# Kernel tuning notes

Hardware: AMD Instinct MI355X
Metric: run time of the kernel (lower is better)

## Reference

```python
import jax, jax.numpy as jnp
import numpy as np

N = 50000      # nodes
M = 600000     # message edges (rows of e2)
E = 1600000    # bond-graph edges
H = 128        # hidden_channels
OE = 256       # out_emb_channels
OC = 1         # out_channels
NL = 3         # num_output_layers
ED = 8         # edge_dim


def _glorot(key, shape):
    fan_in = shape[-1]
    return jax.random.normal(key, shape, jnp.float32) / jnp.sqrt(jnp.float32(fan_in))


def setup_inputs() -> dict:
    key = jax.random.key(0)
    ks = jax.random.split(key, 24)
    inp = {}
    inp["e2"] = jax.random.normal(ks[0], (M, H), jnp.float32)
    inp["i"] = jax.random.randint(ks[1], (M,), 0, N)
    inp["afe"] = jax.random.normal(ks[2], (N, 7), jnp.float32)
    inp["b_edge_index"] = jax.random.randint(ks[3], (2, E), 0, N)
    inp["b_edge_attr"] = jax.random.uniform(ks[4], (E, ED), jnp.float32)
    # lin_v: Linear(H+7, H)
    inp["lin_v_w"] = _glorot(ks[5], (H, H + 7))
    inp["lin_v_b"] = jnp.zeros((H,), jnp.float32)
    # PDNConv (shared across both calls): lin (no bias) + edge MLP 8->8->1
    inp["conv_lin_w"] = _glorot(ks[6], (H, H))
    inp["mlp_w1"] = _glorot(ks[7], (ED, ED))
    inp["mlp_b1"] = jnp.zeros((ED,), jnp.float32)
    inp["mlp_w2"] = _glorot(ks[8], (1, ED))
    inp["mlp_b2"] = jnp.zeros((1,), jnp.float32)
    # lin_up: Linear(H, OE)
    inp["lin_up_w"] = _glorot(ks[9], (OE, H))
    inp["lin_up_b"] = jnp.zeros((OE,), jnp.float32)
    # output MLP stack: NL x Linear(OE, OE)
    inp["lins_w"] = _glorot(ks[10], (NL, OE, OE))
    inp["lins_b"] = jnp.zeros((NL, OE), jnp.float32)
    # final lin: Linear(OE, OC, bias=False)
    inp["lin_w"] = _glorot(ks[11], (OC, OE))
    return inp


def reference(e2, i, afe, b_edge_index, b_edge_attr,
              lin_v_w, lin_v_b, conv_lin_w, mlp_w1, mlp_b1, mlp_w2, mlp_b2,
              lin_up_w, lin_up_b, lins_w, lins_b, lin_w):
    # v = scatter_sum(e2, i) over nodes
    v = jax.ops.segment_sum(e2, i, num_segments=N)          # [N, H]
    v = jnp.concatenate([v, afe], axis=1) @ lin_v_w.T + lin_v_b  # [N, H]

    # PDNConv edge weights (shared by both conv calls): mlp(edge_attr) -> sigmoid scalar
    h = jnp.maximum(b_edge_attr @ mlp_w1.T + mlp_b1, 0.0)
    ew = jax.nn.sigmoid(h @ mlp_w2.T + mlp_b2)[:, 0]        # [E]
    row, col = b_edge_index[0], b_edge_index[1]
    # gcn_norm (no self loops): deg over destination, symmetric normalization
    deg = jax.ops.segment_sum(ew, col, num_segments=N)
    dinv = jnp.where(deg > 0, jax.lax.rsqrt(jnp.maximum(deg, 1e-30)), 0.0)
    norm = dinv[row] * ew * dinv[col]                        # [E]

    def conv(x):
        xw = x @ conv_lin_w.T                                # [N, H]
        return jax.ops.segment_sum(xw[row] * norm[:, None], col, num_segments=N)

    v = conv(v)
    v = conv(v)
    v = jax.nn.relu(v)

    v = v @ lin_up_w.T + lin_up_b                            # [N, OE]
    for l in range(NL):
        v = jax.nn.relu(v @ lins_w[l].T + lins_b[l])
    v = v @ lin_w.T                                          # [N, OC]
    return v
```

## Files before the change

kernel.cpp:

```cpp
#include <hip/hip_runtime.h>


#define Nn 50000
#define Mm 600000
#define Ee 1600000

typedef unsigned short u16;
typedef unsigned int u32;
typedef __attribute__((ext_vector_type(8))) short bh8;
typedef __attribute__((ext_vector_type(4))) float f4;

__device__ __forceinline__ float bf2f(u16 u) {
    union { u32 i; float f; } v; v.i = ((u32)u) << 16; return v.f;
}
__device__ __forceinline__ u16 f2bf(float f) {
    union { float f; u32 u; } v; v.f = f;
    return (u16)((v.u + 0x7fffu + ((v.u >> 16) & 1u)) >> 16);
}

__global__ __launch_bounds__(256) void k_edge(
    const float* __restrict__ attr, const int* __restrict__ eidx,
    const float* __restrict__ w1, const float* __restrict__ b1,
    const float* __restrict__ w2, const float* __restrict__ b2,
    float* __restrict__ ew, float* __restrict__ deg, int* __restrict__ cntC)
{
    __shared__ float sW1[64], sB1[8], sW2[8], sB2;
    int t = threadIdx.x;
    if (t < 64) sW1[t] = w1[t];
    if (t < 8) { sB1[t] = b1[t]; sW2[t] = w2[t]; }
    if (t == 0) sB2 = b2[0];
    __syncthreads();
    int e = blockIdx.x * 256 + t;
    if (e >= Ee) return;
    float4 q0 = *(const float4*)(attr + (size_t)e * 8);
    float4 q1 = *(const float4*)(attr + (size_t)e * 8 + 4);
    float a[8] = { q0.x, q0.y, q0.z, q0.w, q1.x, q1.y, q1.z, q1.w };
    float z = sB2;
#pragma unroll
    for (int j = 0; j < 8; ++j) {
        float h = sB1[j];
#pragma unroll
        for (int k = 0; k < 8; ++k) h += a[k] * sW1[j * 8 + k];
        z += fmaxf(h, 0.f) * sW2[j];
    }
    float s = 1.f / (1.f + __expf(-z));
    ew[e] = s;
    int c = eidx[Ee + e];
    atomicAdd(&deg[c], s);
    atomicAdd(&cntC[c], 1);
}

__global__ __launch_bounds__(256) void k_cntm(const int* __restrict__ ii,
                                              int* __restrict__ cnt)
{
    int m = blockIdx.x * 256 + threadIdx.x;
    if (m < Mm) atomicAdd(&cnt[ii[m]], 1);
}

__device__ void scan_one(const int* __restrict__ cnt, int* __restrict__ off,
                         int* __restrict__ cur, int* buf)
{
    int t = threadIdx.x;
    const int CH = (Nn + 1023) >> 10;
    int lo = t * CH, hi = lo + CH;
    if (hi > Nn) hi = Nn;
    if (lo > Nn) lo = Nn;
    int s = 0;
    for (int i = lo; i < hi; ++i) s += cnt[i];
    __syncthreads();
    buf[t] = s;
    __syncthreads();
    for (int d = 1; d < 1024; d <<= 1) {
        int v = (t >= d) ? buf[t - d] : 0;
        __syncthreads();
        buf[t] += v;
        __syncthreads();
    }
    int base = buf[t] - s;
    for (int i = lo; i < hi; ++i) { off[i] = base; cur[i] = base; base += cnt[i]; }
    if (t == 1023) off[Nn] = buf[1023];
}

__global__ __launch_bounds__(1024) void k_scan(
    const int* __restrict__ cntC, int* __restrict__ offC, int* __restrict__ curC,
    const int* __restrict__ cntM, int* __restrict__ offM, int* __restrict__ curM,
    const float* __restrict__ deg, float* __restrict__ dinv)
{
    __shared__ int buf[1024];
    scan_one(cntC, offC, curC, buf);
    scan_one(cntM, offM, curM, buf);
    for (int n = threadIdx.x; n < Nn; n += 1024) {
        float d = deg[n];
        dinv[n] = (d > 0.f) ? rsqrtf(fmaxf(d, 1e-30f)) : 0.f;
    }
}

__global__ __launch_bounds__(256) void k_scatter_col(
    const int* __restrict__ eidx, const float* __restrict__ ew,
    const float* __restrict__ dinv, int* __restrict__ cur,
    int* __restrict__ rowp, float* __restrict__ normp)
{
    int e = blockIdx.x * 256 + threadIdx.x;
    if (e >= Ee) return;
    int r = eidx[e], c = eidx[Ee + e];
    float nm = dinv[r] * ew[e] * dinv[c];
    int idx = atomicAdd(&cur[c], 1);
    rowp[idx] = r;
    normp[idx] = nm;
}

__global__ __launch_bounds__(256) void k_scatter_m(
    const int* __restrict__ ii, int* __restrict__ cur, int* __restrict__ midx)
{
    int m = blockIdx.x * 256 + threadIdx.x;
    if (m >= Mm) return;
    midx[atomicAdd(&cur[ii[m]], 1)] = m;
}

__global__ __launch_bounds__(64) void k_segsum(
    const int* __restrict__ offM, const int* __restrict__ midx,
    const float* __restrict__ e2, const float* __restrict__ afe,
    float* __restrict__ Xcat)
{
    int n = blockIdx.x, lane = threadIdx.x;
    int j0 = offM[n], j1 = offM[n + 1];
    float a0 = 0.f, a1 = 0.f;
    for (int j = j0; j < j1; ++j) {
        int m = midx[j];
        float2 p = *(const float2*)(e2 + (size_t)m * 128 + lane * 2);
        a0 += p.x; a1 += p.y;
    }
    *(float2*)(Xcat + (size_t)n * 160 + lane * 2) = make_float2(a0, a1);
    if (lane < 32) {
        int ch = 128 + lane;
        float v = (ch < 135) ? afe[(size_t)n * 7 + (ch - 128)] : 0.f;
        Xcat[(size_t)n * 160 + ch] = v;
    }
}

__global__ __launch_bounds__(256) void k_splitw(
    const float* __restrict__ src, u16* __restrict__ h, u16* __restrict__ l,
    int rows, int sc, int dc)
{
    int idx = blockIdx.x * 256 + threadIdx.x;
    if (idx >= rows * dc) return;
    int r = idx / dc, c = idx % dc;
    float x = (c < sc) ? src[(size_t)r * sc + c] : 0.f;
    u16 hh = f2bf(x);
    h[idx] = hh;
    l[idx] = f2bf(x - bf2f(hh));
}

__global__ __launch_bounds__(256) void k_gemm(
    const float* __restrict__ X, const u16* __restrict__ Wh,
    const u16* __restrict__ Wl, const float* __restrict__ bias,
    void* __restrict__ Y, int M, int K, int NO, int flags)
{
    __shared__ __align__(16) u16 Ah[128][40];
    __shared__ __align__(16) u16 Al[128][40];
    __shared__ __align__(16) u16 Bh[128][40];
    __shared__ __align__(16) u16 Bl[128][40];
    const int t = threadIdx.x;
    const int m0 = blockIdx.x * 128, n0 = blockIdx.y * 128;
    const int lane = t & 63, wv = t >> 6;
    const int wm = (wv >> 1) * 64, wn = (wv & 1) * 64;
    const int lr = lane & 15, lq = lane >> 4;
    const int srow = t >> 1, skc = (t & 1) * 16;
    const bool aok = (m0 + srow) < M;
    const float* Xp = X + (size_t)(m0 + srow) * K + skc;
    const u16* Whp = Wh + (size_t)(n0 + srow) * K + skc;
    const u16* Wlp = Wl + (size_t)(n0 + srow) * K + skc;
    f4 acc[4][4] = {};

    for (int k0 = 0; k0 < K; k0 += 32) {
        float av[16];
#pragma unroll
        for (int g = 0; g < 4; ++g) {
            float4 v = make_float4(0.f, 0.f, 0.f, 0.f);
            if (aok) v = *(const float4*)(Xp + k0 + g * 4);
            av[g * 4 + 0] = v.x; av[g * 4 + 1] = v.y;
            av[g * 4 + 2] = v.z; av[g * 4 + 3] = v.w;
        }
        uint4 bh0 = *(const uint4*)(Whp + k0);
        uint4 bh1 = *(const uint4*)(Whp + k0 + 8);
        uint4 bl0 = *(const uint4*)(Wlp + k0);
        uint4 bl1 = *(const uint4*)(Wlp + k0 + 8);
        __syncthreads();
#pragma unroll
        for (int g = 0; g < 4; ++g) {
            union { u16 s[4]; uint2 d; } h, l;
#pragma unroll
            for (int j = 0; j < 4; ++j) {
                float x = av[g * 4 + j];
                u16 hh = f2bf(x);
                h.s[j] = hh; l.s[j] = f2bf(x - bf2f(hh));
            }
            *(uint2*)&Ah[srow][skc + g * 4] = h.d;
            *(uint2*)&Al[srow][skc + g * 4] = l.d;
        }
        *(uint4*)&Bh[srow][skc]     = bh0;
        *(uint4*)&Bh[srow][skc + 8] = bh1;
        *(uint4*)&Bl[srow][skc]     = bl0;
        *(uint4*)&Bl[srow][skc + 8] = bl1;
        __syncthreads();
        bh8 fah[4], fal[4], fbh[4], fbl[4];
#pragma unroll
        for (int i = 0; i < 4; ++i) {
            fah[i] = *(const bh8*)&Ah[wm + i * 16 + lr][lq * 8];
            fal[i] = *(const bh8*)&Al[wm + i * 16 + lr][lq * 8];
            fbh[i] = *(const bh8*)&Bh[wn + i * 16 + lr][lq * 8];
            fbl[i] = *(const bh8*)&Bl[wn + i * 16 + lr][lq * 8];
        }
#pragma unroll
        for (int mi = 0; mi < 4; ++mi)
#pragma unroll
            for (int ni = 0; ni < 4; ++ni) {
                acc[mi][ni] = __builtin_amdgcn_mfma_f32_16x16x32_bf16(
                    fah[mi], fbh[ni], acc[mi][ni], 0, 0, 0);
                acc[mi][ni] = __builtin_amdgcn_mfma_f32_16x16x32_bf16(
                    fal[mi], fbh[ni], acc[mi][ni], 0, 0, 0);
                acc[mi][ni] = __builtin_amdgcn_mfma_f32_16x16x32_bf16(
                    fah[mi], fbl[ni], acc[mi][ni], 0, 0, 0);
            }
    }
#pragma unroll
    for (int ni = 0; ni < 4; ++ni) {
        int gn = n0 + wn + ni * 16 + lr;
        float bv = bias ? bias[gn] : 0.f;
#pragma unroll
        for (int mi = 0; mi < 4; ++mi) {
#pragma unroll
            for (int r = 0; r < 4; ++r) {
                int gm = m0 + wm + mi * 16 + lq * 4 + r;
                if (gm < M) {
                    float v = acc[mi][ni][r] + bv;
                    if (flags & 1) v = fmaxf(v, 0.f);
                    if (flags & 2) ((u16*)Y)[(size_t)gm * NO + gn] = f2bf(v);
                    else           ((float*)Y)[(size_t)gm * NO + gn] = v;
                }
            }
        }
    }
}

__global__ __launch_bounds__(64) void k_gather(
    const int* __restrict__ off, const int* __restrict__ rowp,
    const float* __restrict__ normp, const u16* __restrict__ xw,
    float* __restrict__ out, int relu)
{
    int n = blockIdx.x, lane = threadIdx.x;
    int j0 = off[n], j1 = off[n + 1];
    float a0 = 0.f, a1 = 0.f;
    for (int j = j0; j < j1; ++j) {
        int r = rowp[j];
        float w = normp[j];
        u32 p = *(const u32*)(xw + (size_t)r * 128 + lane * 2);
        a0 += w * bf2f((u16)(p & 0xffff));
        a1 += w * bf2f((u16)(p >> 16));
    }
    if (relu) { a0 = fmaxf(a0, 0.f); a1 = fmaxf(a1, 0.f); }
    *(float2*)(out + (size_t)n * 128 + lane * 2) = make_float2(a0, a1);
}

__global__ __launch_bounds__(256) void k_final(
    const float* __restrict__ S, const float* __restrict__ lw,
    float* __restrict__ out)
{
    __shared__ float w[256];
    int t = threadIdx.x;
    w[t] = lw[t];
    __syncthreads();
    int n = blockIdx.x * 4 + (t >> 6);
    int lane = t & 63;
    if (n >= Nn) return;
    float s = 0.f;
#pragma unroll
    for (int k = 0; k < 4; ++k)
        s += S[(size_t)n * 256 + lane + k * 64] * w[lane + k * 64];
#pragma unroll
    for (int d = 32; d >= 1; d >>= 1) s += __shfl_xor(s, d, 64);
    if (lane == 0) out[n] = s;
}

extern "C" void kernel_launch(void* const* d_in, const int* in_sizes, int n_in,
                              void* d_out, int out_size, void* d_ws, size_t ws_size,
                              hipStream_t stream)
{
    (void)in_sizes; (void)n_in; (void)out_size; (void)ws_size;
    const float* e2       = (const float*)d_in[0];
    const int*   iidx     = (const int*)d_in[1];
    const float* afe      = (const float*)d_in[2];
    const int*   bei      = (const int*)d_in[3];
    const float* battr    = (const float*)d_in[4];
    const float* lin_v_w  = (const float*)d_in[5];
    const float* lin_v_b  = (const float*)d_in[6];
    const float* conv_w   = (const float*)d_in[7];
    const float* w1       = (const float*)d_in[8];
    const float* b1       = (const float*)d_in[9];
    const float* w2       = (const float*)d_in[10];
    const float* b2       = (const float*)d_in[11];
    const float* lin_up_w = (const float*)d_in[12];
    const float* lin_up_b = (const float*)d_in[13];
    const float* lins_w   = (const float*)d_in[14];
    const float* lins_b   = (const float*)d_in[15];
    const float* lin_w    = (const float*)d_in[16];

    char* ws = (char*)d_ws;
    int*   rowp  = (int*)  (ws + 0);
    float* normp = (float*)(ws + 6400000);
    float* Xcat  = (float*)(ws + 12800000);
    float* s0    = (float*)(ws + 12800000);
    float* v1    = (float*)(ws + 64000000);
    u16*   xw    = (u16*)  (ws + 89600000);
    float* s1    = (float*)(ws + 64000000);
    float* ew    = (float*)(ws + 102400000);
    int*   midx  = (int*)  (ws + 108800000);
    int*   cntC  = (int*)  (ws + 115200000);
    int*   cntM  = (int*)  (ws + 115400000);
    float* deg   = (float*)(ws + 115600000);
    int*   offC  = (int*)  (ws + 115800000);
    int*   curC  = (int*)  (ws + 116000256);
    int*   offM  = (int*)  (ws + 116200256);
    int*   curM  = (int*)  (ws + 116400512);
    float* dinv  = (float*)(ws + 116600512);
    u16*   Wh    = (u16*)  (ws + 116800512);
    u16*   Wl    = (u16*)  (ws + 117332992);

    const int oWv = 0, oConv = 20480, oLup = 36864, oLins = 69632;

    hipMemsetAsync(ws + 115200000, 0, 3 * Nn * 4, stream);

    k_edge<<<(Ee + 255) / 256, 256, 0, stream>>>(battr, bei, w1, b1, w2, b2,
                                                 ew, deg, cntC);
    k_cntm<<<(Mm + 255) / 256, 256, 0, stream>>>(iidx, cntM);
    k_scan<<<1, 1024, 0, stream>>>(cntC, offC, curC, cntM, offM, curM, deg, dinv);
    k_scatter_col<<<(Ee + 255) / 256, 256, 0, stream>>>(bei, ew, dinv, curC,
                                                        rowp, normp);
    k_scatter_m<<<(Mm + 255) / 256, 256, 0, stream>>>(iidx, curM, midx);
    k_segsum<<<Nn, 64, 0, stream>>>(offM, midx, e2, afe, Xcat);

    k_splitw<<<(128 * 160 + 255) / 256, 256, 0, stream>>>(
        lin_v_w, Wh + oWv, Wl + oWv, 128, 135, 160);
    k_splitw<<<(128 * 128 + 255) / 256, 256, 0, stream>>>(
        conv_w, Wh + oConv, Wl + oConv, 128, 128, 128);
    k_splitw<<<(256 * 128 + 255) / 256, 256, 0, stream>>>(
        lin_up_w, Wh + oLup, Wl + oLup, 256, 128, 128);
    k_splitw<<<(768 * 256 + 255) / 256, 256, 0, stream>>>(
        lins_w, Wh + oLins, Wl + oLins, 768, 256, 256);

#define GEMM(Xp, WO, Bp, Yp, M_, K_, NO_, FL_)                                \
    k_gemm<<<dim3(((M_) + 127) / 128, (NO_) / 128), 256, 0, stream>>>(        \
        (const float*)(Xp), Wh + (WO), Wl + (WO), (const float*)(Bp),         \
        (void*)(Yp), M_, K_, NO_, FL_)

    GEMM(Xcat, oWv, lin_v_b, v1, Nn, 160, 128, 0);
    GEMM(v1, oConv, nullptr, xw, Nn, 128, 128, 2);
    k_gather<<<Nn, 64, 0, stream>>>(offC, rowp, normp, xw, v1, 0);
    GEMM(v1, oConv, nullptr, xw, Nn, 128, 128, 2);
    k_gather<<<Nn, 64, 0, stream>>>(offC, rowp, normp, xw, v1, 1);
    GEMM(v1, oLup, lin_up_b, s0, Nn, 128, 256, 0);
    GEMM(s0, oLins + 0 * 65536, lins_b + 0,   s1, Nn, 256, 256, 1);
    GEMM(s1, oLins + 1 * 65536, lins_b + 256, s0, Nn, 256, 256, 1);
    GEMM(s0, oLins + 2 * 65536, lins_b + 512, s1, Nn, 256, 256, 1);
    k_final<<<(Nn + 3) / 4, 256, 0, stream>>>(s1, lin_w, (float*)d_out);
#undef GEMM
}
```

Baseline: 1.470 ms.

## Parallelize prefix scan across blocks, pack edge data, prefetch in gathers

Replaces the single-block 1024-thread scan with a three-phase multi-block scan (per-block scan, scan of block partials, add-back), and computes dinv across the grid. Row index and norm are packed into one int2 array so each gather step reads a single 8-byte entry. The segsum and gather kernels now process four nodes per 256-thread block and software-prefetch the next row, overlapping load latency with accumulation. This costs more kernel launches in exchange for removing the serial scan bottleneck and raising memory-level parallelism.

```diff
diff --git a/kernel.cpp b/kernel.cpp
--- a/kernel.cpp
+++ b/kernel.cpp
@@ -4,6 +4,7 @@
 #define Nn 50000
 #define Mm 600000
 #define Ee 1600000
+#define NB 196
 
 typedef unsigned short u16;
 typedef unsigned int u32;
@@ -57,56 +58,72 @@
     if (m < Mm) atomicAdd(&cnt[ii[m]], 1);
 }
 
-__device__ void scan_one(const int* __restrict__ cnt, int* __restrict__ off,
-                         int* __restrict__ cur, int* buf)
-{
+__global__ __launch_bounds__(256) void k_scanA(
+    const int* __restrict__ cnt, int* __restrict__ loc, int* __restrict__ part)
+{
+    __shared__ int buf[256];
+    int t = threadIdx.x, i = blockIdx.x * 256 + t;
+    int v = (i < Nn) ? cnt[i] : 0;
+    buf[t] = v;
+    __syncthreads();
+#pragma unroll
+    for (int d = 1; d < 256; d <<= 1) {
+        int x = (t >= d) ? buf[t - d] : 0;
+        __syncthreads();
+        buf[t] += x;
+        __syncthreads();
+    }
+    if (i < Nn) loc[i] = buf[t] - v;
+    if (t == 255) part[blockIdx.x] = buf[255];
+}
+
+__global__ __launch_bounds__(256) void k_scanB(int* __restrict__ pA,
+                                               int* __restrict__ pB)
+{
+    int* p = blockIdx.x ? pB : pA;
+    __shared__ int buf[256];
     int t = threadIdx.x;
-    const int CH = (Nn + 1023) >> 10;
-    int lo = t * CH, hi = lo + CH;
-    if (hi > Nn) hi = Nn;
-    if (lo > Nn) lo = Nn;
-    int s = 0;
-    for (int i = lo; i < hi; ++i) s += cnt[i];
+    int v = (t < NB) ? p[t] : 0;
+    buf[t] = v;
     __syncthreads();
-    buf[t] = s;
-    __syncthreads();
-    for (int d = 1; d < 1024; d <<= 1) {
-        int v = (t >= d) ? buf[t - d] : 0;
-        __syncthreads();
-        buf[t] += v;
-        __syncthreads();
-    }
-    int base = buf[t] - s;
-    for (int i = lo; i < hi; ++i) { off[i] = base; cur[i] = base; base += cnt[i]; }
-    if (t == 1023) off[Nn] = buf[1023];
-}
-
-__global__ __launch_bounds__(1024) void k_scan(
-    const int* __restrict__ cntC, int* __restrict__ offC, int* __restrict__ curC,
-    const int* __restrict__ cntM, int* __restrict__ offM, int* __restrict__ curM,
+#pragma unroll
+    for (int d = 1; d < 256; d <<= 1) {
+        int x = (t >= d) ? buf[t - d] : 0;
+        __syncthreads();
+        buf[t] += x;
+        __syncthreads();
+    }
+    if (t < NB) p[t] = buf[t] - v;
+}
+
+__global__ __launch_bounds__(256) void k_scanC(
+    const int* __restrict__ cnt, const int* __restrict__ part,
+    int* __restrict__ off, int* __restrict__ cur,
     const float* __restrict__ deg, float* __restrict__ dinv)
 {
-    __shared__ int buf[1024];
-    scan_one(cntC, offC, curC, buf);
-    scan_one(cntM, offM, curM, buf);
-    for (int n = threadIdx.x; n < Nn; n += 1024) {
-        float d = deg[n];
-        dinv[n] = (d > 0.f) ? rsqrtf(fmaxf(d, 1e-30f)) : 0.f;
+    int t = threadIdx.x, i = blockIdx.x * 256 + t;
+    if (i >= Nn) return;
+    int v = off[i] + part[blockIdx.x];
+    off[i] = v;
+    cur[i] = v;
+    if (i == Nn - 1) off[Nn] = v + cnt[i];
+    if (dinv) {
+        float d = deg[i];
+        dinv[i] = (d > 0.f) ? rsqrtf(fmaxf(d, 1e-30f)) : 0.f;
     }
 }
 
 __global__ __launch_bounds__(256) void k_scatter_col(
     const int* __restrict__ eidx, const float* __restrict__ ew,
     const float* __restrict__ dinv, int* __restrict__ cur,
-    int* __restrict__ rowp, float* __restrict__ normp)
+    int2* __restrict__ edgep)
 {
     int e = blockIdx.x * 256 + threadIdx.x;
     if (e >= Ee) return;
     int r = eidx[e], c = eidx[Ee + e];
     float nm = dinv[r] * ew[e] * dinv[c];
     int idx = atomicAdd(&cur[c], 1);
-    rowp[idx] = r;
-    normp[idx] = nm;
+    edgep[idx] = make_int2(r, __float_as_int(nm));
 }
 
 __global__ __launch_bounds__(256) void k_scatter_m(
@@ -117,17 +134,26 @@
     midx[atomicAdd(&cur[ii[m]], 1)] = m;
 }
 
-__global__ __launch_bounds__(64) void k_segsum(
+__global__ __launch_bounds__(256) void k_segsum(
     const int* __restrict__ offM, const int* __restrict__ midx,
     const float* __restrict__ e2, const float* __restrict__ afe,
     float* __restrict__ Xcat)
 {
-    int n = blockIdx.x, lane = threadIdx.x;
+    int wv = threadIdx.x >> 6, lane = threadIdx.x & 63;
+    int n = blockIdx.x * 4 + wv;
+    if (n >= Nn) return;
     int j0 = offM[n], j1 = offM[n + 1];
     float a0 = 0.f, a1 = 0.f;
-    for (int j = j0; j < j1; ++j) {
+    int j = j0;
+    if (j < j1) {
         int m = midx[j];
         float2 p = *(const float2*)(e2 + (size_t)m * 128 + lane * 2);
+        for (++j; j < j1; ++j) {
+            int m2 = midx[j];
+            float2 p2 = *(const float2*)(e2 + (size_t)m2 * 128 + lane * 2);
+            a0 += p.x; a1 += p.y;
+            p = p2;
+        }
         a0 += p.x; a1 += p.y;
     }
     *(float2*)(Xcat + (size_t)n * 160 + lane * 2) = make_float2(a0, a1);
@@ -243,18 +269,28 @@
     }
 }
 
-__global__ __launch_bounds__(64) void k_gather(
-    const int* __restrict__ off, const int* __restrict__ rowp,
-    const float* __restrict__ normp, const u16* __restrict__ xw,
-    float* __restrict__ out, int relu)
-{
-    int n = blockIdx.x, lane = threadIdx.x;
+__global__ __launch_bounds__(256) void k_gather(
+    const int* __restrict__ off, const int2* __restrict__ edgep,
+    const u16* __restrict__ xw, float* __restrict__ out, int relu)
+{
+    int wv = threadIdx.x >> 6, lane = threadIdx.x & 63;
+    int n = blockIdx.x * 4 + wv;
+    if (n >= Nn) return;
     int j0 = off[n], j1 = off[n + 1];
     float a0 = 0.f, a1 = 0.f;
-    for (int j = j0; j < j1; ++j) {
-        int r = rowp[j];
-        float w = normp[j];
-        u32 p = *(const u32*)(xw + (size_t)r * 128 + lane * 2);
+    int j = j0;
+    if (j < j1) {
+        int2 ep = edgep[j];
+        u32 p = *(const u32*)(xw + (size_t)ep.x * 128 + lane * 2);
+        for (++j; j < j1; ++j) {
+            int2 ep2 = edgep[j];
+            u32 p2 = *(const u32*)(xw + (size_t)ep2.x * 128 + lane * 2);
+            float w = __int_as_float(ep.y);
+            a0 += w * bf2f((u16)(p & 0xffff));
+            a1 += w * bf2f((u16)(p >> 16));
+            ep = ep2; p = p2;
+        }
+        float w = __int_as_float(ep.y);
         a0 += w * bf2f((u16)(p & 0xffff));
         a1 += w * bf2f((u16)(p >> 16));
     }
@@ -306,8 +342,7 @@
     const float* lin_w    = (const float*)d_in[16];
 
     char* ws = (char*)d_ws;
-    int*   rowp  = (int*)  (ws + 0);
-    float* normp = (float*)(ws + 6400000);
+    int2*  edgep = (int2*) (ws + 0);
     float* Xcat  = (float*)(ws + 12800000);
     float* s0    = (float*)(ws + 12800000);
     float* v1    = (float*)(ws + 64000000);
@@ -325,6 +360,8 @@
     float* dinv  = (float*)(ws + 116600512);
     u16*   Wh    = (u16*)  (ws + 116800512);
     u16*   Wl    = (u16*)  (ws + 117332992);
+    int*   partC = (int*)  (ws + 117865472);
+    int*   partM = (int*)  (ws + 117866368);
 
     const int oWv = 0, oConv = 20480, oLup = 36864, oLins = 69632;
 
@@ -333,11 +370,15 @@
     k_edge<<<(Ee + 255) / 256, 256, 0, stream>>>(battr, bei, w1, b1, w2, b2,
                                                  ew, deg, cntC);
     k_cntm<<<(Mm + 255) / 256, 256, 0, stream>>>(iidx, cntM);
-    k_scan<<<1, 1024, 0, stream>>>(cntC, offC, curC, cntM, offM, curM, deg, dinv);
+    k_scanA<<<NB, 256, 0, stream>>>(cntC, offC, partC);
+    k_scanA<<<NB, 256, 0, stream>>>(cntM, offM, partM);
+    k_scanB<<<2, 256, 0, stream>>>(partC, partM);
+    k_scanC<<<NB, 256, 0, stream>>>(cntC, partC, offC, curC, deg, dinv);
+    k_scanC<<<NB, 256, 0, stream>>>(cntM, partM, offM, curM, nullptr, nullptr);
     k_scatter_col<<<(Ee + 255) / 256, 256, 0, stream>>>(bei, ew, dinv, curC,
-                                                        rowp, normp);
+                                                        edgep);
     k_scatter_m<<<(Mm + 255) / 256, 256, 0, stream>>>(iidx, curM, midx);
-    k_segsum<<<Nn, 64, 0, stream>>>(offM, midx, e2, afe, Xcat);
+    k_segsum<<<(Nn + 3) / 4, 256, 0, stream>>>(offM, midx, e2, afe, Xcat);
 
     k_splitw<<<(128 * 160 + 255) / 256, 256, 0, stream>>>(
         lin_v_w, Wh + oWv, Wl + oWv, 128, 135, 160);
@@ -355,9 +396,9 @@
 
     GEMM(Xcat, oWv, lin_v_b, v1, Nn, 160, 128, 0);
     GEMM(v1, oConv, nullptr, xw, Nn, 128, 128, 2);
-    k_gather<<<Nn, 64, 0, stream>>>(offC, rowp, normp, xw, v1, 0);
+    k_gather<<<(Nn + 3) / 4, 256, 0, stream>>>(offC, edgep, xw, v1, 0);
     GEMM(v1, oConv, nullptr, xw, Nn, 128, 128, 2);
-    k_gather<<<Nn, 64, 0, stream>>>(offC, rowp, normp, xw, v1, 1);
+    k_gather<<<(Nn + 3) / 4, 256, 0, stream>>>(offC, edgep, xw, v1, 1);
     GEMM(v1, oLup, lin_up_b, s0, Nn, 128, 256, 0);
     GEMM(s0, oLins + 0 * 65536, lins_b + 0,   s1, Nn, 256, 256, 1);
     GEMM(s1, oLins + 1 * 65536, lins_b + 256, s0, Nn, 256, 256, 1);
```

After: 1.235 ms. 16.0% less time.
